# Performance work log

Measured on AMD Instinct MI355X. Metric: run time of the kernel, lower is better.

## Reference

```python
import jax, jax.numpy as jnp
import numpy as np

MUL = 64          # multiplicity of every irrep block
EMB = 64

# --- normalize_function(gelu): scale phi so E[phi(N(0,1))^2] = 1 (e3nn convention) ---
_z = np.linspace(-8.0, 8.0, 4001)
_gauss = np.exp(-0.5 * _z**2) / np.sqrt(2.0 * np.pi)
_PHI_C = float(np.sqrt(np.trapz(np.asarray(jax.nn.gelu(jnp.asarray(_z)))**2 * _gauss, _z)))

# Levi-Civita tensor (real Wigner 3j for 1x1->1 up to normalization)
_eps = np.zeros((3, 3, 3), np.float32)
for (i, j, k), s in {(0,1,2):1,(1,2,0):1,(2,0,1):1,(0,2,1):-1,(2,1,0):-1,(1,0,2):-1}.items():
    _eps[i, j, k] = s
EPS = jnp.asarray(_eps)

INV_SQ3 = 1.0 / np.sqrt(3.0)   # w3j(1,1,0) component (after sqrt(2l3+1) component-norm scaling)
INV_SQ2 = 1.0 / np.sqrt(2.0)   # eps/sqrt(6) * sqrt(3)
ALPHA_01 = 1.0 / np.sqrt(2.0 * MUL * MUL)  # two uvw paths feed outputs 0e and 1o
ALPHA_2  = 1.0 / np.sqrt(1.0 * MUL * MUL)  # one path feeds 1e


def _mlp(x, Ws):
    # haiku Linear(no bias, N(0,1) init), x -> phi(x @ W / sqrt(fan_in)) with normalized phi
    for W in Ws:
        x = jax.nn.gelu(x @ W * (x.shape[-1] ** -0.5)) / _PHI_C
    return x


def setup_inputs() -> dict:
    key = jax.random.key(0)
    ks = jax.random.split(key, 11)
    B = 128
    return {
        "emb": jax.random.normal(ks[0], (B, EMB), jnp.float32),
        "x1": jax.random.normal(ks[1], (B, 4 * MUL), jnp.float32),   # 64x0e + 64x1o
        "x2": jax.random.normal(ks[2], (B, 4 * MUL), jnp.float32),
        "W0": jax.random.normal(ks[3], (EMB, 256), jnp.float32),
        "W1": jax.random.normal(ks[4], (256, 256), jnp.float32),
        "W2": jax.random.normal(ks[5], (256, 64), jnp.float32),
        "P0": jax.random.normal(ks[6], (64, MUL, MUL, MUL), jnp.float32),
        "P1": jax.random.normal(ks[7], (64, MUL, MUL, MUL), jnp.float32),
        "P2": jax.random.normal(ks[8], (64, MUL, MUL, MUL), jnp.float32),
        "P3": jax.random.normal(ks[9], (64, MUL, MUL, MUL), jnp.float32),
        "P4": jax.random.normal(ks[10], (64, MUL, MUL, MUL), jnp.float32),
    }


def reference(emb, x1, x2, W0, W1, W2, P0, P1, P2, P3, P4):
    B = emb.shape[0]
    # MLP -> per-sample weight vector h  [B, 64]
    h = _mlp(emb, (W0, W1, W2))
    hs = h * (h.shape[-1] ** -0.5)  # / sqrt(w.shape[0])
    # per-instruction generated path weights  [B, u, v, w]
    w0, w1, w2, w3, w4 = (jnp.einsum('xuvw,bx->buvw', P, hs) for P in (P0, P1, P2, P3, P4))

    s1, v1 = x1[:, :MUL], x1[:, MUL:].reshape(B, MUL, 3)
    s2, v2 = x2[:, :MUL], x2[:, MUL:].reshape(B, MUL, 3)

    # (0e,0e)->0e and (1o,1o)->0e
    t0 = jnp.einsum('bu,bv,buvw->bw', s1, s2, w0)
    t3 = jnp.einsum('bui,bvi,buvw->bw', v1, v2, w3) * INV_SQ3
    out0 = ALPHA_01 * (t0 + t3)                      # [B, MUL]
    # (0e,1o)->1o and (1o,0e)->1o
    t1 = jnp.einsum('bu,bvj,buvw->bwj', s1, v2, w1)
    t2 = jnp.einsum('bui,bv,buvw->bwi', v1, s2, w2)
    out1 = ALPHA_01 * (t1 + t2)                      # [B, MUL, 3]
    # (1o,1o)->1e  (cross-product path)
    t4 = jnp.einsum('bui,bvj,buvw,ijk->bwk', v1, v2, w4, EPS) * INV_SQ2
    out2 = ALPHA_2 * t4                              # [B, MUL, 3]

    return jnp.concatenate([out0, out1.reshape(B, 3 * MUL), out2.reshape(B, 3 * MUL)], axis=-1)
```

## Files before the change

### kernel.cpp

```cpp
#include <hip/hip_runtime.h>

typedef float v4f __attribute__((ext_vector_type(4)));
typedef short v8s __attribute__((ext_vector_type(8)));

__device__ __forceinline__ unsigned short f2bf_rn(float f) {
  unsigned u = __float_as_uint(f);
  return (unsigned short)((u + 0x7fffu + ((u >> 16) & 1u)) >> 16);
}
__device__ __forceinline__ float bf2f(unsigned short h) {
  return __uint_as_float((unsigned)h << 16);
}
__device__ __forceinline__ unsigned cvt_pk_bf16(float lo, float hi) {
  unsigned r;
  asm("v_cvt_pk_bf16_f32 %0, %1, %2" : "=v"(r) : "v"(lo), "v"(hi));
  return r;
}

__device__ __forceinline__ void barrier_keep_vmcnt() {
  asm volatile("s_waitcnt lgkmcnt(0)" ::: "memory");
  __builtin_amdgcn_s_barrier();
}

__device__ __forceinline__ float gelu_phi(float x) {
  float t = tanhf(0.7978845608f * (x + 0.044715f * x * x * x));
  return 0.5f * x * (1.0f + t) * 1.5338375f;
}

__global__ __launch_bounds__(256) void k_mlp(const float* __restrict__ emb, const float* __restrict__ W0,
                                             const float* __restrict__ W1, const float* __restrict__ W2,
                                             const float* __restrict__ x1, const float* __restrict__ x2,
                                             float* __restrict__ hsT,
                                             unsigned short* __restrict__ s1c, unsigned short* __restrict__ v1c,
                                             unsigned short* __restrict__ s2c, unsigned short* __restrict__ v2c)
{
  const int blk = blockIdx.x, tid = threadIdx.x;
  if (blk < 128) {
    __shared__ float er[64];
    __shared__ float a1[256];
    __shared__ float a2[256];
    __shared__ float r3[4][64];
    const int b = blk;
    if (tid < 64) er[tid] = emb[b * 64 + tid];
    __syncthreads();
    {
      float s = 0.f;
#pragma unroll 8
      for (int x = 0; x < 64; ++x) s += er[x] * W0[x * 256 + tid];
      a1[tid] = gelu_phi(s * 0.125f);
    }
    __syncthreads();
    {
      float s = 0.f;
#pragma unroll 16
      for (int x = 0; x < 256; ++x) s += a1[x] * W1[x * 256 + tid];
      a2[tid] = gelu_phi(s * 0.0625f);
    }
    __syncthreads();
    {
      const int e = tid & 63, q = tid >> 6;
      float s = 0.f;
#pragma unroll 16
      for (int x = q * 64; x < q * 64 + 64; ++x) s += a2[x] * W2[x * 64 + e];
      r3[q][e] = s;
    }
    __syncthreads();
    if (tid < 64) {
      const float s = r3[0][tid] + r3[1][tid] + r3[2][tid] + r3[3][tid];
      hsT[tid * 128 + b] = gelu_phi(s * 0.0625f) * 0.125f;
    }
  } else {
    const int sel = (blk - 128) >> 3;
    const float* xs = sel ? x2 : x1;
    unsigned short* sc = sel ? s2c : s1c;
    unsigned short* vc = sel ? v2c : v1c;
    for (int i = ((blk - 128) & 7) * 256 + tid; i < 32768; i += 2048) {
      if (i < 8192) {
        sc[i] = f2bf_rn(xs[(i >> 6) * 256 + (i & 63)]);
      } else {
        const int t = i - 8192, g = t >> 13, r = t & 8191;
        vc[g * 8192 + r] = f2bf_rn(xs[(r >> 6) * 256 + 64 + (r & 63) * 3 + g]);
      }
    }
  }
}


template<int G>
__device__ __forceinline__ void gemm_body(
    const float* __restrict__ P,
    const unsigned short* __restrict__ f1g,
    const unsigned short* __restrict__ f2g,
    const float* __restrict__ hsT,
    float* __restrict__ partial,
    int c, int csh,
    unsigned short* ldsF1, unsigned* ldsB32)
{
  constexpr int NC  = (G == 0 || G == 3) ? 1 : 3;
  constexpr int NF2 = (G == 0 || G == 2) ? 1 : 3;
  constexpr int NH  = (G == 0 || G == 1) ? 1 : 3;
  constexpr int NCM = (G <= 1) ? 1 : 3;
  constexpr int RB  = (G == 0) ? 0 : (G == 1) ? 128 : (G == 2) ? 512 : (G == 3) ? 896 : 1024;

  const int tid = threadIdx.x;
  const int lane = tid & 63, w = tid >> 6, l16 = lane & 15, quad = lane >> 4;
  const int tq = tid & 15, kp = tid >> 4;
  const int x = c >> (csh - 6);
  const int nsub = 1 << (7 - csh);

  int bidx[2];
  bidx[0] = w * 32 + l16;
  bidx[1] = w * 32 + 16 + l16;

  float hsx[2];
  hsx[0] = hsT[x * 128 + bidx[0]];
  hsx[1] = hsT[x * 128 + bidx[1]];

  v8s fr2[2][NF2][2];
#pragma unroll
  for (int bh = 0; bh < 2; ++bh)
#pragma unroll
    for (int m = 0; m < NF2; ++m)
#pragma unroll
      for (int hh = 0; hh < 2; ++hh)
        fr2[bh][m][hh] = *(const v8s*)(f2g + m * 8192 + bidx[bh] * 64 + hh * 32 + quad * 8);

  v4f acc[2][NC][4];
#pragma unroll
  for (int bh = 0; bh < 2; ++bh)
#pragma unroll
    for (int cc = 0; cc < NC; ++cc)
#pragma unroll
      for (int nf = 0; nf < 4; ++nf) acc[bh][cc][nf] = (v4f){0.f, 0.f, 0.f, 0.f};

  const int swz_w = (((tq & 3) ^ (tq >> 2)) << 2);

  float h[2][NH];

  for (int sub = 0; sub < nsub; ++sub) {
    const int kb = (c << (18 - csh)) + (sub << 11);
    const int u0 = (kb >> 6) & 63;
    __syncthreads();
    {
      const int nchk = NCM * 512;
      for (int i = tid; i < nchk; i += 256) {
        const int uu8 = i & 3, b = (i >> 2) & 127, cm = i >> 9;
        *(v8s*)&ldsF1[(cm * 128 + b) * 40 + uu8 * 8] =
            *(const v8s*)(f1g + cm * 8192 + b * 64 + u0 + uu8 * 8);
      }
    }

    float4 pa0, pa1;
    auto gload = [&](int kk) {
      const float* s = P + (size_t)(kb + kk * 32 + 2 * kp) * 64 + 4 * tq;
      pa0 = *(const float4*)s;
      pa1 = *(const float4*)(s + 64);
    };
    auto bwrite = [&](int buf) {
      unsigned* dst = ldsB32 + (buf * 64 + 4 * tq) * 20 + (kp ^ swz_w);
      dst[0]  = cvt_pk_bf16(pa0.x, pa1.x);
      dst[20] = cvt_pk_bf16(pa0.y, pa1.y);
      dst[40] = cvt_pk_bf16(pa0.z, pa1.z);
      dst[60] = cvt_pk_bf16(pa0.w, pa1.w);
    };

    gload(0);
    bwrite(0);
    gload(1);
    barrier_keep_vmcnt();

#pragma unroll 2
    for (int kk = 0; kk < 64; ++kk) {
      const int buf = kk & 1;
      const int vh = kk & 1;
      v8s bfr[4];
#pragma unroll
      for (int nf = 0; nf < 4; ++nf)
        bfr[nf] = *(const v8s*)&ldsB32[(buf * 64 + nf * 16 + l16) * 20 +
                                       ((quad * 4) ^ ((((l16 >> 2) & 3) ^ nf) << 2))];
      if (vh == 0) {
        const int uu = kk >> 1;
#pragma unroll
        for (int bh = 0; bh < 2; ++bh)
#pragma unroll
          for (int m = 0; m < NH; ++m)
            h[bh][m] = hsx[bh] * bf2f(ldsF1[m * 5120 + bidx[bh] * 40 + uu]);
      }
      if (kk < 63) bwrite(buf ^ 1);
      if (kk < 62) gload(kk + 2);
#pragma unroll
      for (int bh = 0; bh < 2; ++bh) {
#pragma unroll
        for (int cc = 0; cc < NC; ++cc) {
          auto pv = [&](int j) -> float {
            if constexpr (G == 0)
              return h[bh][0] * bf2f((unsigned short)(vh ? fr2[bh][0][1][j] : fr2[bh][0][0][j]));
            else if constexpr (G == 1)
              return h[bh][0] * bf2f((unsigned short)(vh ? fr2[bh][cc][1][j] : fr2[bh][cc][0][j]));
            else if constexpr (G == 2)
              return h[bh][cc] * bf2f((unsigned short)(vh ? fr2[bh][0][1][j] : fr2[bh][0][0][j]));
            else if constexpr (G == 3)
              return h[bh][0] * bf2f((unsigned short)(vh ? fr2[bh][0][1][j] : fr2[bh][0][0][j]))
                   + h[bh][1] * bf2f((unsigned short)(vh ? fr2[bh][1][1][j] : fr2[bh][1][0][j]))
                   + h[bh][2] * bf2f((unsigned short)(vh ? fr2[bh][2][1][j] : fr2[bh][2][0][j]));
            else {
              const int i1 = (cc + 1) % 3, j2 = (cc + 2) % 3;
              return h[bh][i1] * bf2f((unsigned short)(vh ? fr2[bh][j2][1][j] : fr2[bh][j2][0][j]))
                   - h[bh][j2] * bf2f((unsigned short)(vh ? fr2[bh][i1][1][j] : fr2[bh][i1][0][j]));
            }
          };
          v8s af;
          unsigned* a32 = (unsigned*)&af;
#pragma unroll
          for (int t = 0; t < 4; ++t)
            a32[t] = cvt_pk_bf16(pv(2 * t), pv(2 * t + 1));
#pragma unroll
          for (int nf = 0; nf < 4; ++nf)
            acc[bh][cc][nf] = __builtin_amdgcn_mfma_f32_16x16x32_bf16(af, bfr[nf], acc[bh][cc][nf], 0, 0, 0);
        }
      }
      barrier_keep_vmcnt();
    }
  }

#pragma unroll
  for (int bh = 0; bh < 2; ++bh)
#pragma unroll
    for (int cc = 0; cc < NC; ++cc)
#pragma unroll
      for (int nf = 0; nf < 4; ++nf)
#pragma unroll
        for (int r = 0; r < 4; ++r) {
          const int row = RB + cc * 128 + w * 32 + bh * 16 + quad * 4 + r;
          partial[((size_t)c * 1408 + row) * 64 + nf * 16 + l16] = acc[bh][cc][nf][r];
        }
}

__global__ __launch_bounds__(256, 2) void tp_gemm(
    const float* __restrict__ P0, const float* __restrict__ P1, const float* __restrict__ P2,
    const float* __restrict__ P3, const float* __restrict__ P4,
    const unsigned short* __restrict__ s1c, const unsigned short* __restrict__ v1c,
    const unsigned short* __restrict__ s2c, const unsigned short* __restrict__ v2c,
    const float* __restrict__ hsT, float* __restrict__ partial, int csh)
{
  __shared__ __align__(16) unsigned ldsB32[2 * 64 * 20];
  __shared__ __align__(16) unsigned short ldsF1[3 * 128 * 40];
  const int g = blockIdx.x >> csh;
  const int c = blockIdx.x & ((1 << csh) - 1);
  switch (g) {
    case 0: gemm_body<0>(P0, s1c, s2c, hsT, partial, c, csh, ldsF1, ldsB32); break;
    case 1: gemm_body<1>(P1, s1c, v2c, hsT, partial, c, csh, ldsF1, ldsB32); break;
    case 2: gemm_body<2>(P2, v1c, s2c, hsT, partial, c, csh, ldsF1, ldsB32); break;
    case 3: gemm_body<3>(P3, v1c, v2c, hsT, partial, c, csh, ldsF1, ldsB32); break;
    default: gemm_body<4>(P4, v1c, v2c, hsT, partial, c, csh, ldsF1, ldsB32); break;
  }
}

__global__ __launch_bounds__(448) void k_fin(const float* __restrict__ partial, float* __restrict__ out, int nch)
{
  const int b = blockIdx.x, i = threadIdx.x;
  int w, rA, rB;
  if (i < 64)       { w = i; rA = b; rB = 896 + b; }
  else if (i < 256) { const int t = i - 64;  w = t / 3; const int j = t - 3 * w; rA = 128 + j * 128 + b; rB = 512 + j * 128 + b; }
  else              { const int t = i - 256; w = t / 3; const int k = t - 3 * w; rA = 1024 + k * 128 + b; rB = rA; }
  const float* pA = partial + (size_t)rA * 64 + w;
  const float* pB = partial + (size_t)rB * 64 + w;
  float sA = 0.f, sB = 0.f;
#pragma unroll 8
  for (int cc = 0; cc < nch; ++cc) {
    sA += pA[(size_t)cc * 90112];
    sB += pB[(size_t)cc * 90112];
  }
  const float A01 = 0.011048543f;
  const float sc = 0.015625f * 0.70710678f;
  float o;
  if (i < 64)       o = A01 * (sA + 0.57735027f * sB);
  else if (i < 256) o = A01 * (sA + sB);
  else              o = sc * sA;
  out[b * 448 + i] = o;
}

extern "C" void kernel_launch(void* const* d_in, const int* in_sizes, int n_in,
                              void* d_out, int out_size, void* d_ws, size_t ws_size,
                              hipStream_t stream)
{
  const float* emb = (const float*)d_in[0];
  const float* x1  = (const float*)d_in[1];
  const float* x2  = (const float*)d_in[2];
  const float* W0  = (const float*)d_in[3];
  const float* W1  = (const float*)d_in[4];
  const float* W2  = (const float*)d_in[5];
  const float* P0  = (const float*)d_in[6];
  const float* P1  = (const float*)d_in[7];
  const float* P2  = (const float*)d_in[8];
  const float* P3  = (const float*)d_in[9];
  const float* P4  = (const float*)d_in[10];
  float* out = (float*)d_out;
  char* ws = (char*)d_ws;

  float* hsT = (float*)ws;
  unsigned short* s1c = (unsigned short*)(ws + 32768);
  unsigned short* v1c = (unsigned short*)(ws + 49152);
  unsigned short* s2c = (unsigned short*)(ws + 98304);
  unsigned short* v2c = (unsigned short*)(ws + 114688);
  float* partial = (float*)(ws + 163840);

  const int csh = (ws_size >= (size_t)163840 + ((size_t)360448 << 7)) ? 7 : 6;

  k_mlp<<<144, 256, 0, stream>>>(emb, W0, W1, W2, x1, x2, hsT, s1c, v1c, s2c, v2c);
  tp_gemm<<<5 << csh, 256, 0, stream>>>(P0, P1, P2, P3, P4, s1c, v1c, s2c, v2c, hsT, partial, csh);
  k_fin<<<128, 448, 0, stream>>>(partial, out, 1 << csh);
}
```

Before: 497.0 us.

## Split heavy three-component GEMM groups across N halves for load balance

```diff
diff --git a/kernel.cpp b/kernel.cpp
--- a/kernel.cpp
+++ b/kernel.cpp
@@ -9,16 +9,6 @@
 }
 __device__ __forceinline__ float bf2f(unsigned short h) {
   return __uint_as_float((unsigned)h << 16);
-}
-__device__ __forceinline__ unsigned cvt_pk_bf16(float lo, float hi) {
-  unsigned r;
-  asm("v_cvt_pk_bf16_f32 %0, %1, %2" : "=v"(r) : "v"(lo), "v"(hi));
-  return r;
-}
-
-__device__ __forceinline__ void barrier_keep_vmcnt() {
-  asm volatile("s_waitcnt lgkmcnt(0)" ::: "memory");
-  __builtin_amdgcn_s_barrier();
 }
 
 __device__ __forceinline__ float gelu_phi(float x) {
@@ -85,14 +75,14 @@
 }
 
 
-template<int G>
+template<int G, int HALF>
 __device__ __forceinline__ void gemm_body(
     const float* __restrict__ P,
     const unsigned short* __restrict__ f1g,
     const unsigned short* __restrict__ f2g,
     const float* __restrict__ hsT,
     float* __restrict__ partial,
-    int c, int csh,
+    int c, int csh, int nh,
     unsigned short* ldsF1, unsigned* ldsB32)
 {
   constexpr int NC  = (G == 0 || G == 3) ? 1 : 3;
@@ -100,12 +90,17 @@
   constexpr int NH  = (G == 0 || G == 1) ? 1 : 3;
   constexpr int NCM = (G <= 1) ? 1 : 3;
   constexpr int RB  = (G == 0) ? 0 : (G == 1) ? 128 : (G == 2) ? 512 : (G == 3) ? 896 : 1024;
+  constexpr int NF  = HALF ? 2 : 4;
 
   const int tid = threadIdx.x;
   const int lane = tid & 63, w = tid >> 6, l16 = lane & 15, quad = lane >> 4;
-  const int tq = tid & 15, kp = tid >> 4;
   const int x = c >> (csh - 6);
   const int nsub = 1 << (7 - csh);
+  const int n0 = nh * 32;
+
+  const int tq = HALF ? (tid & 7) : (tid & 15);
+  const int kp = HALF ? ((tid >> 3) & 15) : (tid >> 4);
+  const bool stg = HALF ? (tid < 128) : true;
 
   int bidx[2];
   bidx[0] = w * 32 + l16;
@@ -124,15 +119,16 @@
       for (int hh = 0; hh < 2; ++hh)
         fr2[bh][m][hh] = *(const v8s*)(f2g + m * 8192 + bidx[bh] * 64 + hh * 32 + quad * 8);
 
-  v4f acc[2][NC][4];
+  v4f acc[2][NC][NF];
 #pragma unroll
   for (int bh = 0; bh < 2; ++bh)
 #pragma unroll
     for (int cc = 0; cc < NC; ++cc)
 #pragma unroll
-      for (int nf = 0; nf < 4; ++nf) acc[bh][cc][nf] = (v4f){0.f, 0.f, 0.f, 0.f};
-
-  const int swz_w = (((tq & 3) ^ (tq >> 2)) << 2);
+      for (int nf = 0; nf < NF; ++nf) acc[bh][cc][nf] = (v4f){0.f, 0.f, 0.f, 0.f};
+
+  const int swz_w = (tq & 3) << 2;
+  const int swz_r = ((l16 >> 2) & 3) << 2;
 
   float h[2][NH];
 
@@ -151,32 +147,34 @@
 
     float4 pa0, pa1;
     auto gload = [&](int kk) {
-      const float* s = P + (size_t)(kb + kk * 32 + 2 * kp) * 64 + 4 * tq;
+      const float* s = P + (size_t)(kb + kk * 32 + 2 * kp) * 64 + n0 + 4 * tq;
       pa0 = *(const float4*)s;
       pa1 = *(const float4*)(s + 64);
     };
     auto bwrite = [&](int buf) {
-      unsigned* dst = ldsB32 + (buf * 64 + 4 * tq) * 20 + (kp ^ swz_w);
-      dst[0]  = cvt_pk_bf16(pa0.x, pa1.x);
-      dst[20] = cvt_pk_bf16(pa0.y, pa1.y);
-      dst[40] = cvt_pk_bf16(pa0.z, pa1.z);
-      dst[60] = cvt_pk_bf16(pa0.w, pa1.w);
+      unsigned* dst = ldsB32 + (buf * (NF * 16) + 4 * tq) * 20 + (kp ^ swz_w);
+      dst[0]  = (unsigned)f2bf_rn(pa0.x) | ((unsigned)f2bf_rn(pa1.x) << 16);
+      dst[20] = (unsigned)f2bf_rn(pa0.y) | ((unsigned)f2bf_rn(pa1.y) << 16);
+      dst[40] = (unsigned)f2bf_rn(pa0.z) | ((unsigned)f2bf_rn(pa1.z) << 16);
+      dst[60] = (unsigned)f2bf_rn(pa0.w) | ((unsigned)f2bf_rn(pa1.w) << 16);
     };
 
-    gload(0);
-    bwrite(0);
-    gload(1);
-    barrier_keep_vmcnt();
+    if (stg) {
+      gload(0);
+      bwrite(0);
+      gload(1);
+    }
+    __syncthreads();
 
 #pragma unroll 2
     for (int kk = 0; kk < 64; ++kk) {
       const int buf = kk & 1;
       const int vh = kk & 1;
-      v8s bfr[4];
-#pragma unroll
-      for (int nf = 0; nf < 4; ++nf)
-        bfr[nf] = *(const v8s*)&ldsB32[(buf * 64 + nf * 16 + l16) * 20 +
-                                       ((quad * 4) ^ ((((l16 >> 2) & 3) ^ nf) << 2))];
+      v8s bfr[NF];
+#pragma unroll
+      for (int nf = 0; nf < NF; ++nf)
+        bfr[nf] = *(const v8s*)&ldsB32[(buf * (NF * 16) + nf * 16 + l16) * 20 +
+                                       ((quad * 4) ^ swz_r)];
       if (vh == 0) {
         const int uu = kk >> 1;
 #pragma unroll
@@ -185,40 +183,41 @@
           for (int m = 0; m < NH; ++m)
             h[bh][m] = hsx[bh] * bf2f(ldsF1[m * 5120 + bidx[bh] * 40 + uu]);
       }
-      if (kk < 63) bwrite(buf ^ 1);
-      if (kk < 62) gload(kk + 2);
+      if (stg) {
+        if (kk < 63) bwrite(buf ^ 1);
+        if (kk < 62) gload(kk + 2);
+      }
 #pragma unroll
       for (int bh = 0; bh < 2; ++bh) {
 #pragma unroll
         for (int cc = 0; cc < NC; ++cc) {
-          auto pv = [&](int j) -> float {
+          v8s af;
+#pragma unroll
+          for (int j = 0; j < 8; ++j) {
+            float p;
             if constexpr (G == 0)
-              return h[bh][0] * bf2f((unsigned short)(vh ? fr2[bh][0][1][j] : fr2[bh][0][0][j]));
+              p = h[bh][0] * bf2f((unsigned short)fr2[bh][0][vh][j]);
             else if constexpr (G == 1)
-              return h[bh][0] * bf2f((unsigned short)(vh ? fr2[bh][cc][1][j] : fr2[bh][cc][0][j]));
+              p = h[bh][0] * bf2f((unsigned short)fr2[bh][cc][vh][j]);
             else if constexpr (G == 2)
-              return h[bh][cc] * bf2f((unsigned short)(vh ? fr2[bh][0][1][j] : fr2[bh][0][0][j]));
+              p = h[bh][cc] * bf2f((unsigned short)fr2[bh][0][vh][j]);
             else if constexpr (G == 3)
-              return h[bh][0] * bf2f((unsigned short)(vh ? fr2[bh][0][1][j] : fr2[bh][0][0][j]))
-                   + h[bh][1] * bf2f((unsigned short)(vh ? fr2[bh][1][1][j] : fr2[bh][1][0][j]))
-                   + h[bh][2] * bf2f((unsigned short)(vh ? fr2[bh][2][1][j] : fr2[bh][2][0][j]));
+              p = h[bh][0] * bf2f((unsigned short)fr2[bh][0][vh][j])
+                + h[bh][1] * bf2f((unsigned short)fr2[bh][1][vh][j])
+                + h[bh][2] * bf2f((unsigned short)fr2[bh][2][vh][j]);
             else {
               const int i1 = (cc + 1) % 3, j2 = (cc + 2) % 3;
-              return h[bh][i1] * bf2f((unsigned short)(vh ? fr2[bh][j2][1][j] : fr2[bh][j2][0][j]))
-                   - h[bh][j2] * bf2f((unsigned short)(vh ? fr2[bh][i1][1][j] : fr2[bh][i1][0][j]));
+              p = h[bh][i1] * bf2f((unsigned short)fr2[bh][j2][vh][j])
+                - h[bh][j2] * bf2f((unsigned short)fr2[bh][i1][vh][j]);
             }
-          };
-          v8s af;
-          unsigned* a32 = (unsigned*)&af;
-#pragma unroll
-          for (int t = 0; t < 4; ++t)
-            a32[t] = cvt_pk_bf16(pv(2 * t), pv(2 * t + 1));
-#pragma unroll
-          for (int nf = 0; nf < 4; ++nf)
+            af[j] = (short)(__float_as_uint(p) >> 16);
+          }
+#pragma unroll
+          for (int nf = 0; nf < NF; ++nf)
             acc[bh][cc][nf] = __builtin_amdgcn_mfma_f32_16x16x32_bf16(af, bfr[nf], acc[bh][cc][nf], 0, 0, 0);
         }
       }
-      barrier_keep_vmcnt();
+      __syncthreads();
     }
   }
 
@@ -227,11 +226,12 @@
 #pragma unroll
     for (int cc = 0; cc < NC; ++cc)
 #pragma unroll
-      for (int nf = 0; nf < 4; ++nf)
+      for (int nf = 0; nf < NF; ++nf)
 #pragma unroll
         for (int r = 0; r < 4; ++r) {
           const int row = RB + cc * 128 + w * 32 + bh * 16 + quad * 4 + r;
-          partial[((size_t)c * 1408 + row) * 64 + nf * 16 + l16] = acc[bh][cc][nf][r];
+          const int col = n0 + nf * 16 + l16;
+          partial[((size_t)c * 1408 + row) * 64 + col] = acc[bh][cc][nf][r];
         }
 }
 
@@ -244,14 +244,17 @@
 {
   __shared__ __align__(16) unsigned ldsB32[2 * 64 * 20];
   __shared__ __align__(16) unsigned short ldsF1[3 * 128 * 40];
-  const int g = blockIdx.x >> csh;
-  const int c = blockIdx.x & ((1 << csh) - 1);
-  switch (g) {
-    case 0: gemm_body<0>(P0, s1c, s2c, hsT, partial, c, csh, ldsF1, ldsB32); break;
-    case 1: gemm_body<1>(P1, s1c, v2c, hsT, partial, c, csh, ldsF1, ldsB32); break;
-    case 2: gemm_body<2>(P2, v1c, s2c, hsT, partial, c, csh, ldsF1, ldsB32); break;
-    case 3: gemm_body<3>(P3, v1c, v2c, hsT, partial, c, csh, ldsF1, ldsB32); break;
-    default: gemm_body<4>(P4, v1c, v2c, hsT, partial, c, csh, ldsF1, ldsB32); break;
+  const int slot = blockIdx.x & 7;
+  const int c = blockIdx.x >> 3;
+  switch (slot) {
+    case 0:  gemm_body<0, 0>(P0, s1c, s2c, hsT, partial, c, csh, 0, ldsF1, ldsB32); break;
+    case 1:  gemm_body<1, 1>(P1, s1c, v2c, hsT, partial, c, csh, 0, ldsF1, ldsB32); break;
+    case 2:  gemm_body<1, 1>(P1, s1c, v2c, hsT, partial, c, csh, 1, ldsF1, ldsB32); break;
+    case 3:  gemm_body<2, 1>(P2, v1c, s2c, hsT, partial, c, csh, 0, ldsF1, ldsB32); break;
+    case 4:  gemm_body<2, 1>(P2, v1c, s2c, hsT, partial, c, csh, 1, ldsF1, ldsB32); break;
+    case 5:  gemm_body<3, 0>(P3, v1c, v2c, hsT, partial, c, csh, 0, ldsF1, ldsB32); break;
+    case 6:  gemm_body<4, 1>(P4, v1c, v2c, hsT, partial, c, csh, 0, ldsF1, ldsB32); break;
+    default: gemm_body<4, 1>(P4, v1c, v2c, hsT, partial, c, csh, 1, ldsF1, ldsB32); break;
   }
 }
 
@@ -307,6 +310,6 @@
   const int csh = (ws_size >= (size_t)163840 + ((size_t)360448 << 7)) ? 7 : 6;
 
   k_mlp<<<144, 256, 0, stream>>>(emb, W0, W1, W2, x1, x2, hsT, s1c, v1c, s2c, v2c);
-  tp_gemm<<<5 << csh, 256, 0, stream>>>(P0, P1, P2, P3, P4, s1c, v1c, s2c, v2c, hsT, partial, csh);
+  tp_gemm<<<8 << csh, 256, 0, stream>>>(P0, P1, P2, P3, P4, s1c, v1c, s2c, v2c, hsT, partial, csh);
   k_fin<<<128, 448, 0, stream>>>(partial, out, 1 << csh);
 }
```

Result: faster. 420.4 us (-15.4%).
